# Kernel optimization log

Hardware: AMD Instinct MI355X
Metric: run time of the kernel (lower is better)

Reference implementation:

```python
import jax, jax.numpy as jnp
import numpy as np

N_NODES = 100000


def setup_inputs() -> dict:
    key = jax.random.key(0)
    k1, k2, k3 = jax.random.split(key, 3)
    x = jax.random.normal(k1, (N_NODES, 128), dtype=jnp.float32)
    edge_index = jax.random.randint(k2, (2, 1600000), 0, N_NODES, dtype=jnp.int64)
    # GCNConv linear weight (hidden, input) and bias; PReLU slope (init 0.25 as in torch)
    W = jax.random.normal(k3, (128, 128), dtype=jnp.float32) * (1.0 / np.sqrt(128))
    b = jnp.zeros((128,), dtype=jnp.float32)
    prelu_a = jnp.full((1,), 0.25, dtype=jnp.float32)
    return {"x": x, "edge_index": edge_index, "W": W, "b": b, "prelu_a": prelu_a}


def reference(x, edge_index, W, b, prelu_a):
    n = x.shape[0]
    # add self loops (as in forward's add_self_loops)
    loop = jnp.arange(n, dtype=edge_index.dtype)
    src = jnp.concatenate([edge_index[0], loop])  # [E+N]
    dst = jnp.concatenate([edge_index[1], loop])
    # linear transform first (small GEMM), then gather/scatter on hidden dim
    h = x @ W.T  # [N, H]
    # symmetric degree normalization 1/sqrt(deg_src * deg_dst), deg = in-degree incl. self-loop
    ones = jnp.ones_like(dst, dtype=h.dtype)
    deg = jax.ops.segment_sum(ones, dst, num_segments=n)
    dinv = jnp.where(deg > 0, jax.lax.rsqrt(deg), 0.0)  # [N]
    norm = dinv[src] * dinv[dst]  # [E+N]
    msg = h[src] * norm[:, None]  # gather + scale, memory-bound
    out = jax.ops.segment_sum(msg, dst, num_segments=n) + b  # scatter-add
    # PReLU (single shared slope); dropout is identity in eval mode
    out = jnp.where(out >= 0, out, prelu_a[0] * out)
    return out
```

## Files before the change

### kernel.cpp

```cpp
#include <hip/hip_runtime.h>
#include <math.h>

#define HDIM 128
#define BSH 8
#define CAP 5120
#define CH 8192
#define GEMM_BLKS 782

typedef __attribute__((ext_vector_type(8))) short short8;
typedef __attribute__((ext_vector_type(4))) float f32x4;

__device__ inline unsigned short bf16_hi(float f) {
    return (unsigned short)(__float_as_uint(f) >> 16);
}
__device__ inline unsigned short bf16_rn(float f) {
    unsigned int u = __float_as_uint(f);
    return (unsigned short)((u + 0x7FFF + ((u >> 16) & 1)) >> 16);
}

__global__ __launch_bounds__(256) void prep_kernel(
    const float* __restrict__ W, uint4* __restrict__ Whg, uint4* __restrict__ Wlg,
    int* __restrict__ bcur) {
    const int t = threadIdx.x;
    bcur[t] = t * CAP;
    bcur[t + 256] = (t + 256) * CAP;
    for (int idx = t; idx < 2048; idx += 256) {
        const int j = idx >> 4;
        const int c = idx & 15;
        const float4* wp = (const float4*)(W + (size_t)j * HDIM + c * 8);
        float4 va = wp[0], vb = wp[1];
        float vs[8] = {va.x, va.y, va.z, va.w, vb.x, vb.y, vb.z, vb.w};
        unsigned short h[8], l[8];
        #pragma unroll
        for (int k = 0; k < 8; ++k) {
            h[k] = bf16_hi(vs[k]);
            float hf = __uint_as_float((unsigned int)h[k] << 16);
            l[k] = bf16_hi(vs[k] - hf);
        }
        uint4 hch, lch;
        hch.x = (unsigned int)h[0] | ((unsigned int)h[1] << 16);
        hch.y = (unsigned int)h[2] | ((unsigned int)h[3] << 16);
        hch.z = (unsigned int)h[4] | ((unsigned int)h[5] << 16);
        hch.w = (unsigned int)h[6] | ((unsigned int)h[7] << 16);
        lch.x = (unsigned int)l[0] | ((unsigned int)l[1] << 16);
        lch.y = (unsigned int)l[2] | ((unsigned int)l[3] << 16);
        lch.z = (unsigned int)l[4] | ((unsigned int)l[5] << 16);
        lch.w = (unsigned int)l[6] | ((unsigned int)l[7] << 16);
        Whg[idx] = hch;
        Wlg[idx] = lch;
    }
}

__device__ __forceinline__ void gemm_body(
    const float* __restrict__ x, const uint4* __restrict__ Whg,
    const uint4* __restrict__ Wlg, unsigned short* __restrict__ gb, int n,
    int g0, int g1, int bid, int nblk) {
    const int t = threadIdx.x;
    const int wave = t >> 6;
    const int lane = t & 63;
    const int q = lane >> 4;
    const int m = lane & 15;

    for (int grp = g0 + bid; grp < g1; grp += nblk) {
        const int rowbase = (grp << 7) + (wave << 5);

        f32x4 acc[2][8];
        #pragma unroll
        for (int mt = 0; mt < 2; ++mt)
            #pragma unroll
            for (int ct = 0; ct < 8; ++ct)
                acc[mt][ct] = (f32x4){0.f, 0.f, 0.f, 0.f};

        #pragma unroll
        for (int kk = 0; kk < 4; ++kk) {
            short8 ah[2], al[2];
            #pragma unroll
            for (int mt = 0; mt < 2; ++mt) {
                const int r = rowbase + (mt << 4) + m;
                float vs[8];
                if (r < n) {
                    const float4* xp = (const float4*)(x + (size_t)r * HDIM + (kk << 5) + (q << 3));
                    float4 va = xp[0], vb = xp[1];
                    vs[0] = va.x; vs[1] = va.y; vs[2] = va.z; vs[3] = va.w;
                    vs[4] = vb.x; vs[5] = vb.y; vs[6] = vb.z; vs[7] = vb.w;
                } else {
                    #pragma unroll
                    for (int k = 0; k < 8; ++k) vs[k] = 0.f;
                }
                #pragma unroll
                for (int k = 0; k < 8; ++k) {
                    unsigned short h = bf16_hi(vs[k]);
                    float hf = __uint_as_float((unsigned int)h << 16);
                    unsigned short lo = bf16_hi(vs[k] - hf);
                    ah[mt][k] = (short)h;
                    al[mt][k] = (short)lo;
                }
            }
            #pragma unroll
            for (int ct = 0; ct < 8; ++ct) {
                const int nn = (ct << 4) + m;
                const int fidx = (nn << 4) | ((kk << 2) + q);
                short8 bh = *(const short8*)&Whg[fidx];
                short8 bl = *(const short8*)&Wlg[fidx];
                #pragma unroll
                for (int mt = 0; mt < 2; ++mt) {
                    acc[mt][ct] = __builtin_amdgcn_mfma_f32_16x16x32_bf16(ah[mt], bh, acc[mt][ct], 0, 0, 0);
                    acc[mt][ct] = __builtin_amdgcn_mfma_f32_16x16x32_bf16(al[mt], bh, acc[mt][ct], 0, 0, 0);
                    acc[mt][ct] = __builtin_amdgcn_mfma_f32_16x16x32_bf16(ah[mt], bl, acc[mt][ct], 0, 0, 0);
                }
            }
        }

        #pragma unroll
        for (int mt = 0; mt < 2; ++mt) {
            #pragma unroll
            for (int rr = 0; rr < 4; ++rr) {
                const int grow = rowbase + (mt << 4) + (q << 2) + rr;
                if (grow < n) {
                    unsigned short* gp = gb + (size_t)grow * HDIM + m;
                    #pragma unroll
                    for (int ct = 0; ct < 8; ++ct)
                        gp[ct << 4] = bf16_rn(acc[mt][ct][rr]);
                }
            }
        }
    }
}

__device__ __forceinline__ void binB_body(
    const int* __restrict__ ei, int E,
    int* __restrict__ bcur, unsigned int* __restrict__ eb,
    int chunk, int* hist, int* base, int* cur) {
    const int t = threadIdx.x;
    const int c0 = chunk * CH;
    hist[t] = 0;
    hist[t + 256] = 0;
    __syncthreads();

    int sv[CH / 256], dv[CH / 256];
    #pragma unroll
    for (int k = 0; k < CH / 256; ++k) {
        int e = c0 + t + (k << 8);
        if (e < E) {
            sv[k] = ei[e];
            dv[k] = ei[E + e];
            atomicAdd(&hist[dv[k] >> BSH], 1);
        } else {
            dv[k] = -1;
        }
    }
    __syncthreads();
    if (hist[t] > 0)       base[t]       = atomicAdd(&bcur[t],       hist[t]);
    if (hist[t + 256] > 0) base[t + 256] = atomicAdd(&bcur[t + 256], hist[t + 256]);
    cur[t] = 0;
    cur[t + 256] = 0;
    __syncthreads();
    #pragma unroll
    for (int k = 0; k < CH / 256; ++k) {
        if (dv[k] >= 0) {
            int bkt = dv[k] >> BSH;
            int o = atomicAdd(&cur[bkt], 1);
            eb[(size_t)base[bkt] + o] =
                ((unsigned int)(dv[k] & ((1 << BSH) - 1)) << 24) | (unsigned int)sv[k];
        }
    }
}

__global__ __launch_bounds__(256) void fuseAB_kernel(
    const int* __restrict__ ei, int E, int* __restrict__ bcur,
    unsigned int* __restrict__ eb,
    const float* __restrict__ x, const uint4* __restrict__ Whg,
    const uint4* __restrict__ Wlg, unsigned short* __restrict__ gb,
    int n, int nchunk, int ngroups) {
    __shared__ int s_a[512], s_b[512], s_c[512];
    const int bid = blockIdx.x;
    if (bid < nchunk)
        binB_body(ei, E, bcur, eb, bid, s_a, s_b, s_c);
    else
        gemm_body(x, Whg, Wlg, gb, n, 0, ngroups, bid - nchunk, GEMM_BLKS);
}

__global__ __launch_bounds__(512) void binC_kernel(
    const unsigned int* __restrict__ eb, const int* __restrict__ bcur,
    int* __restrict__ row_ptr, float* __restrict__ dinv,
    int* __restrict__ col, int n, int NB) {
    __shared__ int hist[256];
    __shared__ int cur[256];
    __shared__ int red[512];
    __shared__ int wsum[4];
    const int t = threadIdx.x;
    const int b = blockIdx.x;
    const int node0 = b << BSH;
    const size_t s0 = (size_t)b * CAP;
    const int cnt = bcur[b] - b * CAP;

    red[t] = (t < b) ? (bcur[t] - t * CAP) : 0;
    __syncthreads();
    #pragma unroll
    for (int off = 256; off > 0; off >>= 1) {
        if (t < off) red[t] += red[t + off];
        __syncthreads();
    }
    const int o0 = red[0];

    unsigned int r[CAP / 512];
    #pragma unroll
    for (int k = 0; k < CAP / 512; ++k) {
        const int e = t + (k << 9);
        r[k] = (e < cnt) ? eb[s0 + e] : 0u;
    }

    if (t < 256) hist[t] = 0;
    __syncthreads();
    #pragma unroll
    for (int k = 0; k < CAP / 512; ++k) {
        const int e = t + (k << 9);
        if (e < cnt) atomicAdd(&hist[r[k] >> 24], 1);
    }
    __syncthreads();
    const int v = (t < 256) ? hist[t] : 0;
    int x = v;
    #pragma unroll
    for (int off = 1; off < 64; off <<= 1) {
        int u = __shfl_up(x, off);
        if ((t & 63) >= off) x += u;
    }
    if (t < 256 && (t & 63) == 63) wsum[t >> 6] = x;
    __syncthreads();
    if (t < 4) {
        int y = wsum[t];
        #pragma unroll
        for (int off = 1; off < 4; off <<= 1) {
            int u = __shfl_up(y, off);
            if (t >= off) y += u;
        }
        wsum[t] = y;
    }
    __syncthreads();
    if (t < 256) {
        int excl = x - v + ((t >> 6) ? wsum[(t >> 6) - 1] : 0);
        int node = node0 + t;
        if (node < n) {
            row_ptr[node] = o0 + excl;
            dinv[node] = rsqrtf((float)v + 1.0f);
            if (node == n - 1) row_ptr[n] = o0 + excl + v;
        }
        cur[t] = o0 + excl;
    }
    __syncthreads();
    #pragma unroll
    for (int k = 0; k < CAP / 512; ++k) {
        const int e = t + (k << 9);
        if (e < cnt) {
            int pos = atomicAdd(&cur[r[k] >> 24], 1);
            col[pos] = (int)(r[k] & 0xFFFFFF);
        }
    }
}

#define EDGE_ACC(d, u) \
    a[0] = fmaf(d, __uint_as_float((u).x << 16), a[0]); \
    a[1] = fmaf(d, __uint_as_float((u).x & 0xffff0000u), a[1]); \
    a[2] = fmaf(d, __uint_as_float((u).y << 16), a[2]); \
    a[3] = fmaf(d, __uint_as_float((u).y & 0xffff0000u), a[3]); \
    a[4] = fmaf(d, __uint_as_float((u).z << 16), a[4]); \
    a[5] = fmaf(d, __uint_as_float((u).z & 0xffff0000u), a[5]); \
    a[6] = fmaf(d, __uint_as_float((u).w << 16), a[6]); \
    a[7] = fmaf(d, __uint_as_float((u).w & 0xffff0000u), a[7]);

__global__ __launch_bounds__(256) void gather_kernel(
    const int* __restrict__ row_ptr, const int* __restrict__ col,
    const uint4* __restrict__ gbr, const float* __restrict__ dinv,
    const float* __restrict__ bias, const float* __restrict__ prelu_a,
    float* __restrict__ out, int n) {
    const int wv = threadIdx.x >> 6;
    const int lane = threadIdx.x & 63;
    const int q = lane >> 4;
    const int l16 = lane & 15;
    const int i = blockIdx.x * 4 + wv;
    if (i >= n) return;

    const int beg = row_ptr[i];
    const int end = row_ptr[i + 1];
    const float di = dinv[i];

    float a[8];
    #pragma unroll
    for (int k = 0; k < 8; ++k) a[k] = 0.f;

    if (q == 0) {
        uint4 u = gbr[(size_t)i * 16 + l16];
        EDGE_ACC(di, u)
    }

    int e = beg + q;
    for (; e + 12 < end; e += 16) {
        int s0 = col[e];
        int s1 = col[e + 4];
        int s2 = col[e + 8];
        int s3 = col[e + 12];
        float d0 = dinv[s0], d1 = dinv[s1], d2 = dinv[s2], d3 = dinv[s3];
        uint4 u0 = gbr[(size_t)s0 * 16 + l16];
        uint4 u1 = gbr[(size_t)s1 * 16 + l16];
        uint4 u2 = gbr[(size_t)s2 * 16 + l16];
        uint4 u3 = gbr[(size_t)s3 * 16 + l16];
        EDGE_ACC(d0, u0)
        EDGE_ACC(d1, u1)
        EDGE_ACC(d2, u2)
        EDGE_ACC(d3, u3)
    }
    for (; e + 4 < end; e += 8) {
        int s0 = col[e];
        int s1 = col[e + 4];
        float d0 = dinv[s0], d1 = dinv[s1];
        uint4 u0 = gbr[(size_t)s0 * 16 + l16];
        uint4 u1 = gbr[(size_t)s1 * 16 + l16];
        EDGE_ACC(d0, u0)
        EDGE_ACC(d1, u1)
    }
    if (e < end) {
        int s = col[e];
        float d = dinv[s];
        uint4 u = gbr[(size_t)s * 16 + l16];
        EDGE_ACC(d, u)
    }

    #pragma unroll
    for (int k = 0; k < 8; ++k) {
        a[k] += __shfl_xor(a[k], 16);
        a[k] += __shfl_xor(a[k], 32);
    }

    const float aa = prelu_a[0];
    const int c0 = (l16 << 3) + (q << 1);
    float2 bb = *(const float2*)(bias + c0);
    float v0 = di * a[(q << 1) + 0] + bb.x;
    float v1 = di * a[(q << 1) + 1] + bb.y;
    v0 = v0 >= 0.f ? v0 : aa * v0;
    v1 = v1 >= 0.f ? v1 : aa * v1;
    *(float2*)(out + (size_t)i * HDIM + c0) = make_float2(v0, v1);
}

extern "C" void kernel_launch(void* const* d_in, const int* in_sizes, int n_in,
                              void* d_out, int out_size, void* d_ws, size_t ws_size,
                              hipStream_t stream) {
    const float* x  = (const float*)d_in[0];
    const int*   ei = (const int*)d_in[1];
    const float* W  = (const float*)d_in[2];
    const float* b  = (const float*)d_in[3];
    const float* pa = (const float*)d_in[4];

    const int n = in_sizes[0] / HDIM;
    const int E = in_sizes[1] / 2;
    const int NB = (n + (1 << BSH) - 1) >> BSH;
    const int ngroups = (n + 127) >> 7;

    float* out = (float*)d_out;

    unsigned short* gb      = (unsigned short*)d_ws;
    unsigned int*   eb      = (unsigned int*)(gb + (size_t)n * HDIM);
    uint4*          Whg     = (uint4*)(eb + (size_t)NB * CAP);
    uint4*          Wlg     = Whg + 2048;
    float*          dinv    = (float*)(Wlg + 2048);
    int*            row_ptr = (int*)(dinv + n);
    int*            col     = row_ptr + (n + 1);
    int*            bcur    = col + E;

    const int nchunk = (E + CH - 1) / CH;
    prep_kernel<<<1, 256, 0, stream>>>(W, Whg, Wlg, bcur);
    fuseAB_kernel<<<nchunk + GEMM_BLKS, 256, 0, stream>>>(ei, E, bcur, eb, x, Whg, Wlg, gb, n, nchunk, ngroups);
    binC_kernel<<<NB, 512, 0, stream>>>(eb, bcur, row_ptr, dinv, col, n, NB);
    gather_kernel<<<(n + 3) / 4, 256, 0, stream>>>(row_ptr, col, (const uint4*)gb, dinv, b, pa, out, n);
}
```

Before: 242.2 us.

## Replace global bucket atomics with per-chunk offset tables and drop the prep kernel

The binning pass now does a block-local prefix scan of each chunk's bucket histogram. It writes edges into a chunk-contiguous layout and records per-chunk offsets in a table, instead of claiming space with global atomics on shared bucket cursors. The second binning pass rebuilds each bucket by scanning chunk counts and binary-searching, then writes a padded CSR with int2 begin/end pairs that the gather kernel reads in one load. The separate W-splitting prep kernel is removed: each GEMM block recomputes the bf16 hi/lo split itself, and the GEMM block count is lowered. The aim is to cut a kernel launch and global atomic contention, at the cost of redundant W conversion per block and binary-search work in binC.

```diff
diff --git a/kernel.cpp b/kernel.cpp
--- a/kernel.cpp
+++ b/kernel.cpp
@@ -3,9 +3,9 @@
 
 #define HDIM 128
 #define BSH 8
-#define CAP 5120
+#define CAPC 5120
 #define CH 8192
-#define GEMM_BLKS 782
+#define GEMM_BLKS 316
 
 typedef __attribute__((ext_vector_type(8))) short short8;
 typedef __attribute__((ext_vector_type(4))) float f32x4;
@@ -16,39 +16,6 @@
 __device__ inline unsigned short bf16_rn(float f) {
     unsigned int u = __float_as_uint(f);
     return (unsigned short)((u + 0x7FFF + ((u >> 16) & 1)) >> 16);
-}
-
-__global__ __launch_bounds__(256) void prep_kernel(
-    const float* __restrict__ W, uint4* __restrict__ Whg, uint4* __restrict__ Wlg,
-    int* __restrict__ bcur) {
-    const int t = threadIdx.x;
-    bcur[t] = t * CAP;
-    bcur[t + 256] = (t + 256) * CAP;
-    for (int idx = t; idx < 2048; idx += 256) {
-        const int j = idx >> 4;
-        const int c = idx & 15;
-        const float4* wp = (const float4*)(W + (size_t)j * HDIM + c * 8);
-        float4 va = wp[0], vb = wp[1];
-        float vs[8] = {va.x, va.y, va.z, va.w, vb.x, vb.y, vb.z, vb.w};
-        unsigned short h[8], l[8];
-        #pragma unroll
-        for (int k = 0; k < 8; ++k) {
-            h[k] = bf16_hi(vs[k]);
-            float hf = __uint_as_float((unsigned int)h[k] << 16);
-            l[k] = bf16_hi(vs[k] - hf);
-        }
-        uint4 hch, lch;
-        hch.x = (unsigned int)h[0] | ((unsigned int)h[1] << 16);
-        hch.y = (unsigned int)h[2] | ((unsigned int)h[3] << 16);
-        hch.z = (unsigned int)h[4] | ((unsigned int)h[5] << 16);
-        hch.w = (unsigned int)h[6] | ((unsigned int)h[7] << 16);
-        lch.x = (unsigned int)l[0] | ((unsigned int)l[1] << 16);
-        lch.y = (unsigned int)l[2] | ((unsigned int)l[3] << 16);
-        lch.z = (unsigned int)l[4] | ((unsigned int)l[5] << 16);
-        lch.w = (unsigned int)l[6] | ((unsigned int)l[7] << 16);
-        Whg[idx] = hch;
-        Wlg[idx] = lch;
-    }
 }
 
 __device__ __forceinline__ void gemm_body(
@@ -129,8 +96,8 @@
 
 __device__ __forceinline__ void binB_body(
     const int* __restrict__ ei, int E,
-    int* __restrict__ bcur, unsigned int* __restrict__ eb,
-    int chunk, int* hist, int* base, int* cur) {
+    int* __restrict__ off_tab, unsigned int* __restrict__ eb,
+    int chunk, int* hist, int* off, int* cur, int* wsum) {
     const int t = threadIdx.x;
     const int c0 = chunk * CH;
     hist[t] = 0;
@@ -150,108 +117,191 @@
         }
     }
     __syncthreads();
-    if (hist[t] > 0)       base[t]       = atomicAdd(&bcur[t],       hist[t]);
-    if (hist[t + 256] > 0) base[t + 256] = atomicAdd(&bcur[t + 256], hist[t + 256]);
+
+    const int h0 = hist[2 * t];
+    const int h1 = hist[2 * t + 1];
+    const int pair = h0 + h1;
+    int xs = pair;
+    #pragma unroll
+    for (int o = 1; o < 64; o <<= 1) {
+        int u = __shfl_up(xs, o);
+        if ((t & 63) >= o) xs += u;
+    }
+    if ((t & 63) == 63) wsum[t >> 6] = xs;
+    __syncthreads();
+    if (t < 4) {
+        int y = wsum[t];
+        #pragma unroll
+        for (int o = 1; o < 4; o <<= 1) {
+            int u = __shfl_up(y, o);
+            if (t >= o) y += u;
+        }
+        wsum[t] = y;
+    }
+    __syncthreads();
+    const int ex = xs - pair + ((t >> 6) ? wsum[(t >> 6) - 1] : 0);
+    off[2 * t] = ex;
+    off[2 * t + 1] = ex + h0;
+    off_tab[chunk * 512 + 2 * t] = ex;
+    off_tab[chunk * 512 + 2 * t + 1] = ex + h0;
     cur[t] = 0;
     cur[t + 256] = 0;
     __syncthreads();
+
     #pragma unroll
     for (int k = 0; k < CH / 256; ++k) {
         if (dv[k] >= 0) {
             int bkt = dv[k] >> BSH;
             int o = atomicAdd(&cur[bkt], 1);
-            eb[(size_t)base[bkt] + o] =
+            eb[(size_t)c0 + off[bkt] + o] =
                 ((unsigned int)(dv[k] & ((1 << BSH) - 1)) << 24) | (unsigned int)sv[k];
         }
     }
 }
 
 __global__ __launch_bounds__(256) void fuseAB_kernel(
-    const int* __restrict__ ei, int E, int* __restrict__ bcur,
+    const int* __restrict__ ei, int E, int* __restrict__ off_tab,
     unsigned int* __restrict__ eb,
-    const float* __restrict__ x, const uint4* __restrict__ Whg,
-    const uint4* __restrict__ Wlg, unsigned short* __restrict__ gb,
+    const float* __restrict__ x, const float* __restrict__ W,
+    uint4* __restrict__ Whg, uint4* __restrict__ Wlg,
+    unsigned short* __restrict__ gb,
     int n, int nchunk, int ngroups) {
-    __shared__ int s_a[512], s_b[512], s_c[512];
+    __shared__ int s_h[512], s_o[512], s_c[512];
+    __shared__ int s_w[4];
     const int bid = blockIdx.x;
-    if (bid < nchunk)
-        binB_body(ei, E, bcur, eb, bid, s_a, s_b, s_c);
-    else
+    const int t = threadIdx.x;
+    if (bid < nchunk) {
+        binB_body(ei, E, off_tab, eb, bid, s_h, s_o, s_c, s_w);
+    } else {
+        for (int idx = t; idx < 2048; idx += 256) {
+            const int j = idx >> 4;
+            const int c = idx & 15;
+            const float4* wp = (const float4*)(W + (size_t)j * HDIM + c * 8);
+            float4 va = wp[0], vb = wp[1];
+            float vs[8] = {va.x, va.y, va.z, va.w, vb.x, vb.y, vb.z, vb.w};
+            unsigned short h[8], l[8];
+            #pragma unroll
+            for (int k = 0; k < 8; ++k) {
+                h[k] = bf16_hi(vs[k]);
+                float hf = __uint_as_float((unsigned int)h[k] << 16);
+                l[k] = bf16_hi(vs[k] - hf);
+            }
+            uint4 hch, lch;
+            hch.x = (unsigned int)h[0] | ((unsigned int)h[1] << 16);
+            hch.y = (unsigned int)h[2] | ((unsigned int)h[3] << 16);
+            hch.z = (unsigned int)h[4] | ((unsigned int)h[5] << 16);
+            hch.w = (unsigned int)h[6] | ((unsigned int)h[7] << 16);
+            lch.x = (unsigned int)l[0] | ((unsigned int)l[1] << 16);
+            lch.y = (unsigned int)l[2] | ((unsigned int)l[3] << 16);
+            lch.z = (unsigned int)l[4] | ((unsigned int)l[5] << 16);
+            lch.w = (unsigned int)l[6] | ((unsigned int)l[7] << 16);
+            Whg[idx] = hch;
+            Wlg[idx] = lch;
+        }
+        __threadfence_block();
+        __syncthreads();
         gemm_body(x, Whg, Wlg, gb, n, 0, ngroups, bid - nchunk, GEMM_BLKS);
-}
-
-__global__ __launch_bounds__(512) void binC_kernel(
-    const unsigned int* __restrict__ eb, const int* __restrict__ bcur,
-    int* __restrict__ row_ptr, float* __restrict__ dinv,
-    int* __restrict__ col, int n, int NB) {
-    __shared__ int hist[256];
-    __shared__ int cur[256];
-    __shared__ int red[512];
+    }
+}
+
+__global__ __launch_bounds__(256) void binC_kernel(
+    const unsigned int* __restrict__ eb, const int* __restrict__ off_tab,
+    int2* __restrict__ rp, float* __restrict__ dinv,
+    int* __restrict__ col, int n, int nchunk) {
+    __shared__ int soff[256], sstart[256], hist[256], cur[256];
     __shared__ int wsum[4];
+    __shared__ int stot;
     const int t = threadIdx.x;
     const int b = blockIdx.x;
-    const int node0 = b << BSH;
-    const size_t s0 = (size_t)b * CAP;
-    const int cnt = bcur[b] - b * CAP;
-
-    red[t] = (t < b) ? (bcur[t] - t * CAP) : 0;
-    __syncthreads();
-    #pragma unroll
-    for (int off = 256; off > 0; off >>= 1) {
-        if (t < off) red[t] += red[t + off];
-        __syncthreads();
-    }
-    const int o0 = red[0];
-
-    unsigned int r[CAP / 512];
-    #pragma unroll
-    for (int k = 0; k < CAP / 512; ++k) {
-        const int e = t + (k << 9);
-        r[k] = (e < cnt) ? eb[s0 + e] : 0u;
-    }
-
-    if (t < 256) hist[t] = 0;
-    __syncthreads();
-    #pragma unroll
-    for (int k = 0; k < CAP / 512; ++k) {
-        const int e = t + (k << 9);
-        if (e < cnt) atomicAdd(&hist[r[k] >> 24], 1);
-    }
-    __syncthreads();
-    const int v = (t < 256) ? hist[t] : 0;
-    int x = v;
-    #pragma unroll
-    for (int off = 1; off < 64; off <<= 1) {
-        int u = __shfl_up(x, off);
-        if ((t & 63) >= off) x += u;
-    }
-    if (t < 256 && (t & 63) == 63) wsum[t >> 6] = x;
+
+    int off_c = 0, cnt_c = 0;
+    if (t < nchunk) {
+        off_c = off_tab[t * 512 + b];
+        cnt_c = off_tab[t * 512 + b + 1] - off_c;
+    }
+    soff[t] = off_c;
+
+    int xs = cnt_c;
+    #pragma unroll
+    for (int o = 1; o < 64; o <<= 1) {
+        int u = __shfl_up(xs, o);
+        if ((t & 63) >= o) xs += u;
+    }
+    if ((t & 63) == 63) wsum[t >> 6] = xs;
     __syncthreads();
     if (t < 4) {
         int y = wsum[t];
         #pragma unroll
-        for (int off = 1; off < 4; off <<= 1) {
-            int u = __shfl_up(y, off);
-            if (t >= off) y += u;
+        for (int o = 1; o < 4; o <<= 1) {
+            int u = __shfl_up(y, o);
+            if (t >= o) y += u;
         }
         wsum[t] = y;
     }
     __syncthreads();
-    if (t < 256) {
-        int excl = x - v + ((t >> 6) ? wsum[(t >> 6) - 1] : 0);
-        int node = node0 + t;
-        if (node < n) {
-            row_ptr[node] = o0 + excl;
-            dinv[node] = rsqrtf((float)v + 1.0f);
-            if (node == n - 1) row_ptr[n] = o0 + excl + v;
-        }
-        cur[t] = o0 + excl;
-    }
-    __syncthreads();
-    #pragma unroll
-    for (int k = 0; k < CAP / 512; ++k) {
-        const int e = t + (k << 9);
-        if (e < cnt) {
+    const int exs = xs - cnt_c + ((t >> 6) ? wsum[(t >> 6) - 1] : 0);
+    sstart[t] = exs;
+    if (t == 255) stot = exs + cnt_c;
+    __syncthreads();
+    const int cnt_b = stot;
+
+    unsigned int r[CAPC / 256];
+    #pragma unroll
+    for (int k = 0; k < CAPC / 256; ++k) {
+        const int i = t + (k << 8);
+        unsigned int v = 0u;
+        if (i < cnt_b) {
+            int lo = 0, hi = nchunk - 1;
+            while (lo < hi) {
+                int mid = (lo + hi + 1) >> 1;
+                if (sstart[mid] <= i) lo = mid; else hi = mid - 1;
+            }
+            v = eb[(size_t)lo * CH + soff[lo] + (i - sstart[lo])];
+        }
+        r[k] = v;
+    }
+
+    hist[t] = 0;
+    __syncthreads();
+    #pragma unroll
+    for (int k = 0; k < CAPC / 256; ++k) {
+        const int i = t + (k << 8);
+        if (i < cnt_b) atomicAdd(&hist[r[k] >> 24], 1);
+    }
+    __syncthreads();
+    const int v = hist[t];
+    int ys = v;
+    #pragma unroll
+    for (int o = 1; o < 64; o <<= 1) {
+        int u = __shfl_up(ys, o);
+        if ((t & 63) >= o) ys += u;
+    }
+    if ((t & 63) == 63) wsum[t >> 6] = ys;
+    __syncthreads();
+    if (t < 4) {
+        int y = wsum[t];
+        #pragma unroll
+        for (int o = 1; o < 4; o <<= 1) {
+            int u = __shfl_up(y, o);
+            if (t >= o) y += u;
+        }
+        wsum[t] = y;
+    }
+    __syncthreads();
+    const int excl = ys - v + ((t >> 6) ? wsum[(t >> 6) - 1] : 0);
+
+    const int base = b * CAPC + excl;
+    const int node = (b << BSH) + t;
+    if (node < n) {
+        rp[node] = make_int2(base, base + v);
+        dinv[node] = rsqrtf((float)v + 1.0f);
+    }
+    cur[t] = base;
+    __syncthreads();
+    #pragma unroll
+    for (int k = 0; k < CAPC / 256; ++k) {
+        const int i = t + (k << 8);
+        if (i < cnt_b) {
             int pos = atomicAdd(&cur[r[k] >> 24], 1);
             col[pos] = (int)(r[k] & 0xFFFFFF);
         }
@@ -269,7 +319,7 @@
     a[7] = fmaf(d, __uint_as_float((u).w & 0xffff0000u), a[7]);
 
 __global__ __launch_bounds__(256) void gather_kernel(
-    const int* __restrict__ row_ptr, const int* __restrict__ col,
+    const int2* __restrict__ rp, const int* __restrict__ col,
     const uint4* __restrict__ gbr, const float* __restrict__ dinv,
     const float* __restrict__ bias, const float* __restrict__ prelu_a,
     float* __restrict__ out, int n) {
@@ -280,8 +330,9 @@
     const int i = blockIdx.x * 4 + wv;
     if (i >= n) return;
 
-    const int beg = row_ptr[i];
-    const int end = row_ptr[i + 1];
+    const int2 be = rp[i];
+    const int beg = be.x;
+    const int end = be.y;
     const float di = dinv[i];
 
     float a[8];
@@ -354,21 +405,21 @@
     const int E = in_sizes[1] / 2;
     const int NB = (n + (1 << BSH) - 1) >> BSH;
     const int ngroups = (n + 127) >> 7;
+    const int nchunk = (E + CH - 1) / CH;
 
     float* out = (float*)d_out;
 
     unsigned short* gb      = (unsigned short*)d_ws;
     unsigned int*   eb      = (unsigned int*)(gb + (size_t)n * HDIM);
-    uint4*          Whg     = (uint4*)(eb + (size_t)NB * CAP);
+    int*            col     = (int*)(eb + (size_t)E);
+    uint4*          Whg     = (uint4*)(col + (size_t)NB * CAPC);
     uint4*          Wlg     = Whg + 2048;
-    float*          dinv    = (float*)(Wlg + 2048);
-    int*            row_ptr = (int*)(dinv + n);
-    int*            col     = row_ptr + (n + 1);
-    int*            bcur    = col + E;
-
-    const int nchunk = (E + CH - 1) / CH;
-    prep_kernel<<<1, 256, 0, stream>>>(W, Whg, Wlg, bcur);
-    fuseAB_kernel<<<nchunk + GEMM_BLKS, 256, 0, stream>>>(ei, E, bcur, eb, x, Whg, Wlg, gb, n, nchunk, ngroups);
-    binC_kernel<<<NB, 512, 0, stream>>>(eb, bcur, row_ptr, dinv, col, n, NB);
-    gather_kernel<<<(n + 3) / 4, 256, 0, stream>>>(row_ptr, col, (const uint4*)gb, dinv, b, pa, out, n);
-}
+    int2*           rp      = (int2*)(Wlg + 2048);
+    float*          dinv    = (float*)(rp + n);
+    int*            off_tab = (int*)(dinv + n);
+
+    fuseAB_kernel<<<nchunk + GEMM_BLKS, 256, 0, stream>>>(
+        ei, E, off_tab, eb, x, W, Whg, Wlg, gb, n, nchunk, ngroups);
+    binC_kernel<<<NB, 256, 0, stream>>>(eb, off_tab, rp, dinv, col, n, nchunk);
+    gather_kernel<<<(n + 3) / 4, 256, 0, stream>>>(rp, col, (const uint4*)gb, dinv, b, pa, out, n);
+}
```

Measured after the change: 236.4 us. 2.4% less time.
